# Kernel tuning notes

Hardware: AMD Instinct MI355X
Metric: run time of the kernel (lower is better)

Reference implementation:

```python
import jax, jax.numpy as jnp
import numpy as np

DT_RANK = 64
N_STATES = 16


def selective_scan(u, delta, A, B, C, D):
    # u,delta: [b,l,d]; A: [d,n]; B,C: [b,l,n]; D: [d]
    dA = jnp.einsum('bld,dn->bldn', delta, A)
    dB_u = jnp.einsum('bld,bld,bln->bldn', delta, u, B)
    # shifted exclusive suffix-sum: cum[t] = sum_{s=t+1}^{L-1} dA[s]
    dA_shift = jnp.concatenate([dA[:, 1:], jnp.zeros_like(dA[:, :1])], axis=1)
    dA_cumsum = jnp.exp(jnp.flip(jnp.cumsum(jnp.flip(dA_shift, axis=1), axis=1), axis=1))
    xs = jnp.cumsum(dB_u * dA_cumsum, axis=1) / (dA_cumsum + 1e-12)
    y = jnp.einsum('bldn,bln->bld', xs, C)
    return y + u * D


def setup_inputs() -> dict:
    key = jax.random.key(0)
    ks = jax.random.split(key, 6)
    b, l, d = 2, 1024, 1024
    dt_rank, n = DT_RANK, N_STATES
    x = jax.random.normal(ks[0], (b, l, d), dtype=jnp.float32)
    # Dense kernels with glorot-ish scale
    W_x = jax.random.normal(ks[1], (d, dt_rank + 2 * n), dtype=jnp.float32) * (1.0 / np.sqrt(d))
    W_dt = jax.random.normal(ks[2], (dt_rank, d), dtype=jnp.float32) * (1.0 / np.sqrt(dt_rank))
    b_dt = jnp.zeros((d,), dtype=jnp.float32)
    # A_log = log(repeat(1..n, d)) as in S6.__init__
    A_log = jnp.log(jnp.tile(jnp.arange(1, n + 1, dtype=jnp.float32)[None, :], (d, 1)))
    D = jnp.ones((d,), dtype=jnp.float32)
    W_out = jax.random.normal(ks[3], (d, d), dtype=jnp.float32) * (1.0 / np.sqrt(d))
    b_out = jnp.zeros((d,), dtype=jnp.float32)
    return {"x": x, "W_x": W_x, "W_dt": W_dt, "b_dt": b_dt,
            "A_log": A_log, "D": D, "W_out": W_out, "b_out": b_out}


def reference(x, W_x, W_dt, b_dt, A_log, D, W_out, b_out):
    n = A_log.shape[1]
    A = -jnp.exp(A_log)                     # [d,n]
    x_dbl = jnp.einsum('bld,de->ble', x, W_x)  # [b,l,dt_rank+2n]
    delta = x_dbl[..., :DT_RANK]
    B = x_dbl[..., DT_RANK:DT_RANK + n]
    C = x_dbl[..., DT_RANK + n:]
    delta = jax.nn.softplus(jnp.einsum('blr,rd->bld', delta, W_dt) + b_dt)
    y = selective_scan(x, delta, A, B, C, D)
    return jnp.einsum('bld,de->ble', y, W_out) + b_out
```

## Files before the change

kernel.cpp:

```cpp
#include <hip/hip_runtime.h>
#include <hip/hip_bf16.h>

#define LSEQ 1024
#define DMODEL 1024
#define NSTATE 16
#define DTRANK 64
#define ECOL 96
#define MTOT 2048

typedef short s16x8 __attribute__((ext_vector_type(8)));
typedef float f32x4 __attribute__((ext_vector_type(4)));

__device__ inline unsigned short f2bf(float f) {
    unsigned int u = __builtin_bit_cast(unsigned int, f);
    u += 0x7FFFu + ((u >> 16) & 1u);
    return (unsigned short)(u >> 16);
}
__device__ inline float bf2f(unsigned short h) {
    unsigned int u = ((unsigned int)h) << 16;
    return __builtin_bit_cast(float, u);
}

__device__ inline f32x4 shflup4(f32x4 v, int off) {
    f32x4 r;
    r[0] = __shfl_up(v[0], off, 64);
    r[1] = __shfl_up(v[1], off, 64);
    r[2] = __shfl_up(v[2], off, 64);
    r[3] = __shfl_up(v[3], off, 64);
    return r;
}

__global__ __launch_bounds__(256) void k_prep(const float* __restrict__ x,
                                              const float* __restrict__ Wx,
                                              const float* __restrict__ Wdt,
                                              const float* __restrict__ Wout,
                                              float* __restrict__ xT,
                                              unsigned short* __restrict__ xh,
                                              unsigned short* __restrict__ xl,
                                              unsigned short* __restrict__ WxTh,
                                              unsigned short* __restrict__ WxTl,
                                              unsigned short* __restrict__ WdtTh,
                                              unsigned short* __restrict__ WdtTl,
                                              unsigned short* __restrict__ WbfT) {
    __shared__ float t[64][65];
    int id = blockIdx.x;
    int tid = threadIdx.x;
    if (id < 512) {
        int d0 = (id & 15) * 64, m0 = (id >> 4) * 64;
        int tx = tid & 63, ty = tid >> 6;
#pragma unroll
        for (int j = 0; j < 64; j += 4) {
            size_t src = (size_t)(m0 + ty + j) * 1024 + d0 + tx;
            float v = x[src];
            t[ty + j][tx] = v;
            unsigned short h = f2bf(v);
            xh[src] = h;
            xl[src] = f2bf(v - bf2f(h));
        }
        __syncthreads();
#pragma unroll
        for (int j = 0; j < 64; j += 4)
            xT[(size_t)(d0 + ty + j) * 2048 + m0 + tx] = t[tx][ty + j];
    } else if (id < 512 + 96) {
        int id2 = id - 512;
        int e0 = (id2 % 3) * 32, k0 = (id2 / 3) * 32;
        int tx = tid & 31, ty = tid >> 5;
#pragma unroll
        for (int j = 0; j < 32; j += 8)
            t[ty + j][tx] = Wx[(size_t)(k0 + ty + j) * 96 + e0 + tx];
        __syncthreads();
#pragma unroll
        for (int j = 0; j < 32; j += 8) {
            float v = t[tx][ty + j];
            unsigned short h = f2bf(v);
            WxTh[(size_t)(e0 + ty + j) * 1024 + k0 + tx] = h;
            WxTl[(size_t)(e0 + ty + j) * 1024 + k0 + tx] = f2bf(v - bf2f(h));
        }
    } else if (id < 512 + 96 + 64) {
        int id3 = id - (512 + 96);
        int d0 = (id3 & 31) * 32, r0 = (id3 >> 5) * 32;
        int tx = tid & 31, ty = tid >> 5;
#pragma unroll
        for (int j = 0; j < 32; j += 8)
            t[ty + j][tx] = Wdt[(size_t)(r0 + ty + j) * 1024 + d0 + tx];
        __syncthreads();
#pragma unroll
        for (int j = 0; j < 32; j += 8) {
            float v = t[tx][ty + j];
            unsigned short h = f2bf(v);
            WdtTh[(size_t)(d0 + ty + j) * 64 + r0 + tx] = h;
            WdtTl[(size_t)(d0 + ty + j) * 64 + r0 + tx] = f2bf(v - bf2f(h));
        }
    } else {
        int id4 = id - (512 + 96 + 64);
        int e0 = (id4 & 15) * 64, k0 = (id4 >> 4) * 64;
        int tx = tid & 63, ty = tid >> 6;
#pragma unroll
        for (int j = 0; j < 64; j += 4)
            t[ty + j][tx] = Wout[(size_t)(k0 + ty + j) * 1024 + e0 + tx];
        __syncthreads();
#pragma unroll
        for (int j = 0; j < 64; j += 4)
            WbfT[(size_t)(e0 + ty + j) * 1024 + k0 + tx] = f2bf(t[tx][ty + j]);
    }
}

__global__ __launch_bounds__(256) void k_xdbl3(const unsigned short* __restrict__ xh,
                                               const unsigned short* __restrict__ xl,
                                               const unsigned short* __restrict__ WxTh,
                                               const unsigned short* __restrict__ WxTl,
                                               float* __restrict__ part) {
    __shared__ unsigned short Ah[32 * 64], Al[32 * 64];
    __shared__ unsigned short Bh[96 * 64], Bl[96 * 64];
    int bm = (blockIdx.x >> 2) * 32;
    int slice = blockIdx.x & 3;
    int tid = threadIdx.x, lane = tid & 63, w = tid >> 6;
    int wm = w >> 1, wn = w & 1;
    int r = lane & 15, kb = lane >> 4;

    f32x4 acc[3];
#pragma unroll
    for (int nf = 0; nf < 3; ++nf) acc[nf] = (f32x4){0.f, 0.f, 0.f, 0.f};

#pragma unroll 1
    for (int kc = 0; kc < 4; ++kc) {
        int kbase = slice * 256 + kc * 64;
        __syncthreads();
        {
            int row = tid >> 3, cc = tid & 7;
            size_t src = (size_t)(bm + row) * 1024 + kbase + cc * 8;
            int dstB = row * 128 + ((cc * 16) ^ ((row & 7) << 4));
            *(s16x8*)((char*)Ah + dstB) = *(const s16x8*)&xh[src];
            *(s16x8*)((char*)Al + dstB) = *(const s16x8*)&xl[src];
        }
#pragma unroll
        for (int j = 0; j < 3; ++j) {
            int c = tid + j * 256;
            int row = c >> 3, cc = c & 7;
            size_t src = (size_t)row * 1024 + kbase + cc * 8;
            int dstB = row * 128 + ((cc * 16) ^ ((row & 7) << 4));
            *(s16x8*)((char*)Bh + dstB) = *(const s16x8*)&WxTh[src];
            *(s16x8*)((char*)Bl + dstB) = *(const s16x8*)&WxTl[src];
        }
        __syncthreads();
#pragma unroll
        for (int ks = 0; ks < 2; ++ks) {
            int sw = (ks * 64 + kb * 16) ^ ((r & 7) << 4);
            s16x8 a_h = *(const s16x8*)((char*)Ah + (wm * 16 + r) * 128 + sw);
            s16x8 a_l = *(const s16x8*)((char*)Al + (wm * 16 + r) * 128 + sw);
#pragma unroll
            for (int nf = 0; nf < 3; ++nf) {
                int brow = wn * 48 + nf * 16 + r;
                s16x8 b_h = *(const s16x8*)((char*)Bh + brow * 128 + sw);
                s16x8 b_l = *(const s16x8*)((char*)Bl + brow * 128 + sw);
                acc[nf] = __builtin_amdgcn_mfma_f32_16x16x32_bf16(a_h, b_h, acc[nf], 0, 0, 0);
                acc[nf] = __builtin_amdgcn_mfma_f32_16x16x32_bf16(a_h, b_l, acc[nf], 0, 0, 0);
                acc[nf] = __builtin_amdgcn_mfma_f32_16x16x32_bf16(a_l, b_h, acc[nf], 0, 0, 0);
            }
        }
    }
    float* pb = part + (size_t)slice * 2048 * 96;
#pragma unroll
    for (int nf = 0; nf < 3; ++nf)
#pragma unroll
        for (int j = 0; j < 4; ++j)
            pb[(size_t)(bm + wm * 16 + kb * 4 + j) * 96 + wn * 48 + nf * 16 + r] = acc[nf][j];
}

__global__ __launch_bounds__(256) void k_delta2(const float* __restrict__ part,
                                                const unsigned short* __restrict__ WdtTh,
                                                const unsigned short* __restrict__ WdtTl,
                                                const float* __restrict__ bdt,
                                                float* __restrict__ deltaT,
                                                float* __restrict__ bpk,
                                                float* __restrict__ cpk) {
    __shared__ char pool[34816];
    unsigned short* Ah = (unsigned short*)pool;
    unsigned short* Al = (unsigned short*)(pool + 16384);
    float (*slab)[32][68] = (float (*)[32][68])pool;

    int bm = blockIdx.y * 128;
    int bn = blockIdx.x * 64;
    int tid = threadIdx.x, lane = tid & 63, w = tid >> 6;
    int wm = w >> 1, wn = w & 1;
    int r = lane & 15, kb = lane >> 4;

#pragma unroll
    for (int i = 0; i < 8; ++i) {
        int q = tid + i * 256;
        int row = q >> 4, c4 = q & 15;
        size_t off = (size_t)(bm + row) * 96 + c4 * 4;
        f32x4 v = *(const f32x4*)&part[off];
#pragma unroll
        for (int s = 1; s < 4; ++s) v += *(const f32x4*)&part[(size_t)s * 2048 * 96 + off];
        ushort4 h4, l4;
        h4.x = f2bf(v[0]); l4.x = f2bf(v[0] - bf2f(h4.x));
        h4.y = f2bf(v[1]); l4.y = f2bf(v[1] - bf2f(h4.y));
        h4.z = f2bf(v[2]); l4.z = f2bf(v[2] - bf2f(h4.z));
        h4.w = f2bf(v[3]); l4.w = f2bf(v[3] - bf2f(h4.w));
        int dstB = row * 128 + ((c4 * 8) ^ ((row & 7) << 4));
        *(ushort4*)((char*)Ah + dstB) = h4;
        *(ushort4*)((char*)Al + dstB) = l4;
    }
    if (blockIdx.x == 0) {
#pragma unroll
        for (int i = 0; i < 4; ++i) {
            int q = tid + i * 256;
            int row = q >> 3, c4 = q & 7;
            size_t off = (size_t)(bm + row) * 96 + 64 + c4 * 4;
            f32x4 v = *(const f32x4*)&part[off];
#pragma unroll
            for (int s = 1; s < 4; ++s) v += *(const f32x4*)&part[(size_t)s * 2048 * 96 + off];
            if (c4 < 4) *(f32x4*)&bpk[(size_t)(bm + row) * 16 + c4 * 4] = v;
            else        *(f32x4*)&cpk[(size_t)(bm + row) * 16 + (c4 - 4) * 4] = v;
        }
    }
    __syncthreads();

    f32x4 acc[4][2];
#pragma unroll
    for (int mf = 0; mf < 4; ++mf)
#pragma unroll
        for (int nf = 0; nf < 2; ++nf) acc[mf][nf] = (f32x4){0.f, 0.f, 0.f, 0.f};

#pragma unroll
    for (int ks = 0; ks < 2; ++ks) {
        int sw = (ks * 64 + kb * 16) ^ ((r & 7) << 4);
        s16x8 Afh[4], Afl[4], Bh[2], Bl[2];
#pragma unroll
        for (int mf = 0; mf < 4; ++mf) {
            int arow = wm * 64 + mf * 16 + r;
            Afh[mf] = *(const s16x8*)((char*)Ah + arow * 128 + sw);
            Afl[mf] = *(const s16x8*)((char*)Al + arow * 128 + sw);
        }
#pragma unroll
        for (int nf = 0; nf < 2; ++nf) {
            size_t b = (size_t)(bn + wn * 32 + nf * 16 + r) * 64 + ks * 32 + kb * 8;
            Bh[nf] = *(const s16x8*)&WdtTh[b];
            Bl[nf] = *(const s16x8*)&WdtTl[b];
        }
#pragma unroll
        for (int mf = 0; mf < 4; ++mf)
#pragma unroll
            for (int nf = 0; nf < 2; ++nf) {
                acc[mf][nf] = __builtin_amdgcn_mfma_f32_16x16x32_bf16(Afh[mf], Bh[nf], acc[mf][nf], 0, 0, 0);
                acc[mf][nf] = __builtin_amdgcn_mfma_f32_16x16x32_bf16(Afh[mf], Bl[nf], acc[mf][nf], 0, 0, 0);
                acc[mf][nf] = __builtin_amdgcn_mfma_f32_16x16x32_bf16(Afl[mf], Bh[nf], acc[mf][nf], 0, 0, 0);
            }
    }
    __syncthreads();

#pragma unroll
    for (int nf = 0; nf < 2; ++nf) {
        float bb = bdt[bn + wn * 32 + nf * 16 + r];
#pragma unroll
        for (int mf = 0; mf < 4; ++mf)
#pragma unroll
            for (int j = 0; j < 4; ++j) {
                float z = acc[mf][nf][j] + bb;
                float sp = fmaxf(z, 0.f) + log1pf(expf(-fabsf(z)));
                slab[w][nf * 16 + r][mf * 16 + kb * 4 + j] = sp;
            }
    }
#pragma unroll
    for (int i = 0; i < 8; ++i) {
        int idx = i * 64 + lane;
        int dl = idx >> 4, mq = (idx & 15) * 4;
        f32x4 v = *(const f32x4*)&slab[w][dl][mq];
        *(f32x4*)&deltaT[(size_t)(bn + wn * 32 + dl) * MTOT + bm + wm * 64 + mq] = v;
    }
}

__global__ __launch_bounds__(256) void k_scan3(const float* __restrict__ deltaT,
                                               const float* __restrict__ xT,
                                               const float* __restrict__ bpk,
                                               const float* __restrict__ cpk,
                                               const float* __restrict__ Alog,
                                               const float* __restrict__ Dp,
                                               unsigned short* __restrict__ yTbf) {
    __shared__ double csum[64];
    __shared__ double Rbef[64];
    __shared__ float TcL[64 * 20];
    __shared__ float syp[64 * 17];

    int tid = threadIdx.x;
    int c = tid >> 2, l = tid & 3;
    int w = tid >> 6, lane = tid & 63;
    int d = blockIdx.x & 1023, b = blockIdx.x >> 10;
    int m0 = b * 1024;

    const f32x4* dp = (const f32x4*)(deltaT + (size_t)d * MTOT + m0 + c * 16);
    const f32x4* up = (const f32x4*)(xT + (size_t)d * MTOT + m0 + c * 16);
    const f32x4* Bp = (const f32x4*)bpk + (size_t)(m0 + c * 16) * 4 + l;
    const f32x4* Cp = (const f32x4*)cpk + (size_t)(m0 + c * 16) * 4 + l;

    double dsum = 0.0;
#pragma unroll
    for (int i = 0; i < 4; ++i) {
        f32x4 v = dp[i];
        dsum += (double)v[0] + (double)v[1] + (double)v[2] + (double)v[3];
    }
    if (l == 0) csum[c] = dsum;
    __syncthreads();
    if (tid < 64) {
        double v = csum[tid];
#pragma unroll
        for (int off = 1; off < 64; off <<= 1) {
            double t = __shfl_down(v, off, 64);
            if (tid + off < 64) v += t;
        }
        Rbef[tid] = v;
    }
    __syncthreads();

    float Af[4], Sb[4];
    double Rb = Rbef[c];
#pragma unroll
    for (int j = 0; j < 4; ++j) {
        Af[j] = -__expf(Alog[d * NSTATE + 4 * l + j]);
        Sb[j] = (float)((double)Af[j] * Rb);
    }
    float Dv = Dp[d];

    float P = 0.f;
    f32x4 Tn = {0.f, 0.f, 0.f, 0.f};
#pragma unroll 1
    for (int t4 = 0; t4 < 4; ++t4) {
        f32x4 rdv = dp[t4];
        f32x4 ruv = up[t4];
        f32x4 Bq0 = Bp[(t4 * 4 + 0) * 4];
        f32x4 Bq1 = Bp[(t4 * 4 + 1) * 4];
        f32x4 Bq2 = Bp[(t4 * 4 + 2) * 4];
        f32x4 Bq3 = Bp[(t4 * 4 + 3) * 4];
        f32x4 Bq[4] = {Bq0, Bq1, Bq2, Bq3};
#pragma unroll
        for (int k = 0; k < 4; ++k) {
            float dlt = rdv[k];
            P += dlt;
            float du = dlt * ruv[k];
#pragma unroll
            for (int j = 0; j < 4; ++j) {
                float e = __expf(fmaf(-Af[j], P, Sb[j]));
                Tn[j] = fmaf(du * Bq[k][j], e, Tn[j]);
            }
        }
    }
    *(f32x4*)&TcL[c * 20 + 4 * l] = Tn;
    __syncthreads();

    {
        f32x4 v = *(const f32x4*)&TcL[lane * 20 + 4 * w];
#pragma unroll
        for (int off = 1; off < 64; off <<= 1) {
            f32x4 t = shflup4(v, off);
            if (lane >= off) v += t;
        }
        f32x4 ex = shflup4(v, 1);
        if (lane == 0) ex = (f32x4){0.f, 0.f, 0.f, 0.f};
        *(f32x4*)&TcL[lane * 20 + 4 * w] = ex;
    }
    __syncthreads();
    f32x4 num = *(const f32x4*)&TcL[c * 20 + 4 * l];

    P = 0.f;
#pragma unroll 1
    for (int t4 = 0; t4 < 4; ++t4) {
        f32x4 rdv = dp[t4];
        f32x4 ruv = up[t4];
        f32x4 Bq[4], Cq[4];
#pragma unroll
        for (int k = 0; k < 4; ++k) {
            Bq[k] = Bp[(t4 * 4 + k) * 4];
            Cq[k] = Cp[(t4 * 4 + k) * 4];
        }
#pragma unroll
        for (int k = 0; k < 4; ++k) {
            float dlt = rdv[k];
            P += dlt;
            float du = dlt * ruv[k];
            float psum = 0.f;
#pragma unroll
            for (int j = 0; j < 4; ++j) {
                float e = __expf(fmaf(-Af[j], P, Sb[j]));
                num[j] = fmaf(du * Bq[k][j], e, num[j]);
                float rr = __builtin_amdgcn_rcpf(e + 1e-12f);
                psum = fmaf(num[j] * rr, Cq[k][j], psum);
            }
            psum += __shfl_xor(psum, 1);
            psum += __shfl_xor(psum, 2);
            if (l == 0) syp[c * 17 + t4 * 4 + k] = fmaf(ruv[k], Dv, psum);
        }
    }
    __syncthreads();
    {
        int cc = tid >> 2, oo = (tid & 3) * 4;
        const float* sp = &syp[cc * 17 + oo];
        ushort4 o;
        o.x = f2bf(sp[0]);
        o.y = f2bf(sp[1]);
        o.z = f2bf(sp[2]);
        o.w = f2bf(sp[3]);
        *reinterpret_cast<ushort4*>(&yTbf[(size_t)d * MTOT + m0 + tid * 4]) = o;
    }
}

__global__ __launch_bounds__(256) void k_ytr(const unsigned short* __restrict__ in,
                                             unsigned short* __restrict__ out) {
    __shared__ unsigned short t[64][66];
    int d0 = blockIdx.y * 64, m0 = blockIdx.x * 64;
    int tx = threadIdx.x & 63, ty = threadIdx.x >> 6;
#pragma unroll
    for (int j = 0; j < 64; j += 4)
        t[ty + j][tx] = in[(size_t)(d0 + ty + j) * MTOT + m0 + tx];
    __syncthreads();
#pragma unroll
    for (int j = 0; j < 64; j += 4)
        out[(size_t)(m0 + ty + j) * 1024 + d0 + tx] = t[tx][ty + j];
}

__global__ __launch_bounds__(256) void k_gemm(const unsigned short* __restrict__ A,
                                              const unsigned short* __restrict__ B,
                                              const float* __restrict__ bias,
                                              float* __restrict__ out) {
    __shared__ unsigned short As[64 * 64];
    __shared__ unsigned short Bs[64 * 64];
    const int GN = 1024, GK = 1024;
    int bm = blockIdx.y * 64;
    int bn = blockIdx.x * 64;
    int tid = threadIdx.x;
    int lane = tid & 63;
    int w = tid >> 6;
    int wm = w >> 1, wn = w & 1;
    int r = lane & 15, kb = lane >> 4;

    f32x4 acc[2][2];
#pragma unroll
    for (int mf = 0; mf < 2; ++mf)
#pragma unroll
        for (int nf = 0; nf < 2; ++nf) acc[mf][nf] = (f32x4){0.f, 0.f, 0.f, 0.f};

    s16x8 ra[2], rb[2];
    auto stage_load = [&](int k0) {
#pragma unroll
        for (int i = 0; i < 2; ++i) {
            int q = tid + i * 256;
            ra[i] = *reinterpret_cast<const s16x8*>(&A[(size_t)(bm + (q >> 3)) * GK + k0 + (q & 7) * 8]);
            rb[i] = *reinterpret_cast<const s16x8*>(&B[(size_t)(bn + (q >> 3)) * GK + k0 + (q & 7) * 8]);
        }
    };

    stage_load(0);
    for (int k0 = 0; k0 < GK; k0 += 64) {
        __syncthreads();
#pragma unroll
        for (int i = 0; i < 2; ++i) {
            int q = tid + i * 256;
            int row = q >> 3;
            int dstB = row * 128 + (((q & 7) * 16) ^ ((row & 7) << 4));
            *(s16x8*)((char*)As + dstB) = ra[i];
            *(s16x8*)((char*)Bs + dstB) = rb[i];
        }
        __syncthreads();
        if (k0 + 64 < GK) stage_load(k0 + 64);
#pragma unroll
        for (int ks = 0; ks < 2; ++ks) {
            int sw = (ks * 64 + kb * 16) ^ ((r & 7) << 4);
            s16x8 af[2], bfr[2];
#pragma unroll
            for (int mf = 0; mf < 2; ++mf)
                af[mf] = *(const s16x8*)((char*)As + (wm * 32 + mf * 16 + r) * 128 + sw);
#pragma unroll
            for (int nf = 0; nf < 2; ++nf)
                bfr[nf] = *(const s16x8*)((char*)Bs + (wn * 32 + nf * 16 + r) * 128 + sw);
#pragma unroll
            for (int mf = 0; mf < 2; ++mf)
#pragma unroll
                for (int nf = 0; nf < 2; ++nf)
                    acc[mf][nf] = __builtin_amdgcn_mfma_f32_16x16x32_bf16(af[mf], bfr[nf], acc[mf][nf], 0, 0, 0);
        }
    }
#pragma unroll
    for (int nf = 0; nf < 2; ++nf) {
        float bb = bias[bn + wn * 32 + nf * 16 + r];
#pragma unroll
        for (int mf = 0; mf < 2; ++mf)
#pragma unroll
            for (int j = 0; j < 4; ++j)
                out[(size_t)(bm + wm * 32 + mf * 16 + kb * 4 + j) * GN + bn + wn * 32 + nf * 16 + r] =
                    acc[mf][nf][j] + bb;
    }
}

extern "C" void kernel_launch(void* const* d_in, const int* in_sizes, int n_in,
                              void* d_out, int out_size, void* d_ws, size_t ws_size,
                              hipStream_t stream) {
    const float* x    = (const float*)d_in[0];
    const float* Wx   = (const float*)d_in[1];
    const float* Wdt  = (const float*)d_in[2];
    const float* bdt  = (const float*)d_in[3];
    const float* Alog = (const float*)d_in[4];
    const float* Dp   = (const float*)d_in[5];
    const float* Wout = (const float*)d_in[6];
    const float* bout = (const float*)d_in[7];
    float* out = (float*)d_out;

    float* xT     = (float*)d_ws;
    float* deltaT = xT + 1024 * 2048;
    float* bpk    = deltaT + 1024 * 2048;
    float* cpk    = bpk + 2048 * 16;
    float* part   = cpk + 2048 * 16;
    unsigned short* xh    = (unsigned short*)(part + 4 * 2048 * 96);
    unsigned short* xl    = xh + 2048 * 1024;
    unsigned short* WxTh  = xl + 2048 * 1024;
    unsigned short* WxTl  = WxTh + 96 * 1024;
    unsigned short* WdtTh = WxTl + 96 * 1024;
    unsigned short* WdtTl = WdtTh + 1024 * 64;
    unsigned short* yTbf  = WdtTl + 1024 * 64;
    unsigned short* ybf   = yTbf + 1024 * 2048;
    unsigned short* WbfT  = ybf + 2048 * 1024;

    k_prep<<<928, 256, 0, stream>>>(x, Wx, Wdt, Wout, xT, xh, xl,
                                    WxTh, WxTl, WdtTh, WdtTl, WbfT);
    k_xdbl3<<<256, 256, 0, stream>>>(xh, xl, WxTh, WxTl, part);
    k_delta2<<<dim3(16, 16), 256, 0, stream>>>(part, WdtTh, WdtTl, bdt, deltaT, bpk, cpk);
    k_scan3<<<2048, 256, 0, stream>>>(deltaT, xT, bpk, cpk, Alog, Dp, yTbf);
    k_ytr<<<dim3(32, 16), 256, 0, stream>>>(yTbf, ybf);
    k_gemm<<<dim3(16, 32), 256, 0, stream>>>(ybf, WbfT, bout, out);
}
```

Before: 72.13 us.

## Process four channels per scan block, store transposed x as bf16, split x on the fly

```diff
diff --git a/kernel.cpp b/kernel.cpp
--- a/kernel.cpp
+++ b/kernel.cpp
@@ -34,9 +34,7 @@
                                               const float* __restrict__ Wx,
                                               const float* __restrict__ Wdt,
                                               const float* __restrict__ Wout,
-                                              float* __restrict__ xT,
-                                              unsigned short* __restrict__ xh,
-                                              unsigned short* __restrict__ xl,
+                                              unsigned short* __restrict__ xTbf,
                                               unsigned short* __restrict__ WxTh,
                                               unsigned short* __restrict__ WxTl,
                                               unsigned short* __restrict__ WdtTh,
@@ -49,18 +47,12 @@
         int d0 = (id & 15) * 64, m0 = (id >> 4) * 64;
         int tx = tid & 63, ty = tid >> 6;
 #pragma unroll
-        for (int j = 0; j < 64; j += 4) {
-            size_t src = (size_t)(m0 + ty + j) * 1024 + d0 + tx;
-            float v = x[src];
-            t[ty + j][tx] = v;
-            unsigned short h = f2bf(v);
-            xh[src] = h;
-            xl[src] = f2bf(v - bf2f(h));
-        }
-        __syncthreads();
-#pragma unroll
         for (int j = 0; j < 64; j += 4)
-            xT[(size_t)(d0 + ty + j) * 2048 + m0 + tx] = t[tx][ty + j];
+            t[ty + j][tx] = x[(size_t)(m0 + ty + j) * 1024 + d0 + tx];
+        __syncthreads();
+#pragma unroll
+        for (int j = 0; j < 64; j += 4)
+            xTbf[(size_t)(d0 + ty + j) * 2048 + m0 + tx] = f2bf(t[tx][ty + j]);
     } else if (id < 512 + 96) {
         int id2 = id - 512;
         int e0 = (id2 % 3) * 32, k0 = (id2 / 3) * 32;
@@ -105,8 +97,7 @@
     }
 }
 
-__global__ __launch_bounds__(256) void k_xdbl3(const unsigned short* __restrict__ xh,
-                                               const unsigned short* __restrict__ xl,
+__global__ __launch_bounds__(256) void k_xdbl3(const float* __restrict__ x,
                                                const unsigned short* __restrict__ WxTh,
                                                const unsigned short* __restrict__ WxTl,
                                                float* __restrict__ part) {
@@ -129,9 +120,19 @@
         {
             int row = tid >> 3, cc = tid & 7;
             size_t src = (size_t)(bm + row) * 1024 + kbase + cc * 8;
+            float4 v0 = *(const float4*)&x[src];
+            float4 v1 = *(const float4*)&x[src + 4];
+            float vv[8] = {v0.x, v0.y, v0.z, v0.w, v1.x, v1.y, v1.z, v1.w};
+            s16x8 h, lo;
+#pragma unroll
+            for (int j = 0; j < 8; ++j) {
+                unsigned short hb = f2bf(vv[j]);
+                h[j] = (short)hb;
+                lo[j] = (short)f2bf(vv[j] - bf2f(hb));
+            }
             int dstB = row * 128 + ((cc * 16) ^ ((row & 7) << 4));
-            *(s16x8*)((char*)Ah + dstB) = *(const s16x8*)&xh[src];
-            *(s16x8*)((char*)Al + dstB) = *(const s16x8*)&xl[src];
+            *(s16x8*)((char*)Ah + dstB) = h;
+            *(s16x8*)((char*)Al + dstB) = lo;
         }
 #pragma unroll
         for (int j = 0; j < 3; ++j) {
@@ -271,85 +272,108 @@
     }
 }
 
-__global__ __launch_bounds__(256) void k_scan3(const float* __restrict__ deltaT,
-                                               const float* __restrict__ xT,
+__global__ __launch_bounds__(256) void k_scan4(const float* __restrict__ deltaT,
+                                               const unsigned short* __restrict__ xTbf,
                                                const float* __restrict__ bpk,
                                                const float* __restrict__ cpk,
                                                const float* __restrict__ Alog,
                                                const float* __restrict__ Dp,
                                                unsigned short* __restrict__ yTbf) {
-    __shared__ double csum[64];
-    __shared__ double Rbef[64];
-    __shared__ float TcL[64 * 20];
-    __shared__ float syp[64 * 17];
+    __shared__ double csum[64][4];
+    __shared__ double Rbef[64][4];
+    __shared__ float TcL[64][4][4][4];
+    __shared__ float syp[4][64 * 17];
 
     int tid = threadIdx.x;
     int c = tid >> 2, l = tid & 3;
     int w = tid >> 6, lane = tid & 63;
-    int d = blockIdx.x & 1023, b = blockIdx.x >> 10;
+    int dgrp = blockIdx.x & 255, b = blockIdx.x >> 8;
+    int d0 = dgrp * 4;
     int m0 = b * 1024;
 
-    const f32x4* dp = (const f32x4*)(deltaT + (size_t)d * MTOT + m0 + c * 16);
-    const f32x4* up = (const f32x4*)(xT + (size_t)d * MTOT + m0 + c * 16);
+    const f32x4* dp[4];
+    const unsigned short* up[4];
+#pragma unroll
+    for (int dg = 0; dg < 4; ++dg) {
+        dp[dg] = (const f32x4*)(deltaT + (size_t)(d0 + dg) * MTOT + m0 + c * 16);
+        up[dg] = xTbf + (size_t)(d0 + dg) * MTOT + m0 + c * 16;
+    }
+
+#pragma unroll
+    for (int dg = 0; dg < 4; ++dg) {
+        double s = 0.0;
+#pragma unroll
+        for (int i = 0; i < 4; ++i) {
+            f32x4 v = dp[dg][i];
+            s += (double)v[0] + (double)v[1] + (double)v[2] + (double)v[3];
+        }
+        if (l == 0) csum[c][dg] = s;
+    }
+    __syncthreads();
+    {
+        double v = csum[lane][w];
+#pragma unroll
+        for (int off = 1; off < 64; off <<= 1) {
+            double t = __shfl_down(v, off, 64);
+            if (lane + off < 64) v += t;
+        }
+        Rbef[lane][w] = v;
+    }
+    __syncthreads();
+
+    float Af[4][4], Sb[4][4];
+#pragma unroll
+    for (int dg = 0; dg < 4; ++dg) {
+        double Rb = Rbef[c][dg];
+#pragma unroll
+        for (int j = 0; j < 4; ++j) {
+            Af[dg][j] = -__expf(Alog[(d0 + dg) * NSTATE + 4 * l + j]);
+            Sb[dg][j] = (float)((double)Af[dg][j] * Rb);
+        }
+    }
+
     const f32x4* Bp = (const f32x4*)bpk + (size_t)(m0 + c * 16) * 4 + l;
     const f32x4* Cp = (const f32x4*)cpk + (size_t)(m0 + c * 16) * 4 + l;
 
-    double dsum = 0.0;
-#pragma unroll
-    for (int i = 0; i < 4; ++i) {
-        f32x4 v = dp[i];
-        dsum += (double)v[0] + (double)v[1] + (double)v[2] + (double)v[3];
-    }
-    if (l == 0) csum[c] = dsum;
-    __syncthreads();
-    if (tid < 64) {
-        double v = csum[tid];
-#pragma unroll
-        for (int off = 1; off < 64; off <<= 1) {
-            double t = __shfl_down(v, off, 64);
-            if (tid + off < 64) v += t;
-        }
-        Rbef[tid] = v;
-    }
-    __syncthreads();
-
-    float Af[4], Sb[4];
-    double Rb = Rbef[c];
-#pragma unroll
-    for (int j = 0; j < 4; ++j) {
-        Af[j] = -__expf(Alog[d * NSTATE + 4 * l + j]);
-        Sb[j] = (float)((double)Af[j] * Rb);
-    }
-    float Dv = Dp[d];
-
-    float P = 0.f;
-    f32x4 Tn = {0.f, 0.f, 0.f, 0.f};
+    float P[4] = {0.f, 0.f, 0.f, 0.f};
+    f32x4 Tn[4];
+#pragma unroll
+    for (int dg = 0; dg < 4; ++dg) Tn[dg] = (f32x4){0.f, 0.f, 0.f, 0.f};
 #pragma unroll 1
     for (int t4 = 0; t4 < 4; ++t4) {
-        f32x4 rdv = dp[t4];
-        f32x4 ruv = up[t4];
-        f32x4 Bq0 = Bp[(t4 * 4 + 0) * 4];
-        f32x4 Bq1 = Bp[(t4 * 4 + 1) * 4];
-        f32x4 Bq2 = Bp[(t4 * 4 + 2) * 4];
-        f32x4 Bq3 = Bp[(t4 * 4 + 3) * 4];
-        f32x4 Bq[4] = {Bq0, Bq1, Bq2, Bq3};
-#pragma unroll
-        for (int k = 0; k < 4; ++k) {
-            float dlt = rdv[k];
-            P += dlt;
-            float du = dlt * ruv[k];
-#pragma unroll
-            for (int j = 0; j < 4; ++j) {
-                float e = __expf(fmaf(-Af[j], P, Sb[j]));
-                Tn[j] = fmaf(du * Bq[k][j], e, Tn[j]);
-            }
-        }
-    }
-    *(f32x4*)&TcL[c * 20 + 4 * l] = Tn;
-    __syncthreads();
-
-    {
-        f32x4 v = *(const f32x4*)&TcL[lane * 20 + 4 * w];
+        f32x4 Bq[4];
+#pragma unroll
+        for (int k = 0; k < 4; ++k) Bq[k] = Bp[(t4 * 4 + k) * 4];
+        f32x4 rdv[4];
+        float ru[4][4];
+#pragma unroll
+        for (int dg = 0; dg < 4; ++dg) {
+            rdv[dg] = dp[dg][t4];
+            ushort4 uv = *(const ushort4*)(up[dg] + t4 * 4);
+            ru[dg][0] = bf2f(uv.x); ru[dg][1] = bf2f(uv.y);
+            ru[dg][2] = bf2f(uv.z); ru[dg][3] = bf2f(uv.w);
+        }
+#pragma unroll
+        for (int k = 0; k < 4; ++k)
+#pragma unroll
+            for (int dg = 0; dg < 4; ++dg) {
+                float dlt = rdv[dg][k];
+                P[dg] += dlt;
+                float du = dlt * ru[dg][k];
+#pragma unroll
+                for (int j = 0; j < 4; ++j) {
+                    float e = __expf(fmaf(-Af[dg][j], P[dg], Sb[dg][j]));
+                    Tn[dg][j] = fmaf(du * Bq[k][j], e, Tn[dg][j]);
+                }
+            }
+    }
+#pragma unroll
+    for (int dg = 0; dg < 4; ++dg) *(f32x4*)&TcL[c][dg][l][0] = Tn[dg];
+    __syncthreads();
+
+#pragma unroll
+    for (int l2 = 0; l2 < 4; ++l2) {
+        f32x4 v = *(const f32x4*)&TcL[lane][w][l2][0];
 #pragma unroll
         for (int off = 1; off < 64; off <<= 1) {
             f32x4 t = shflup4(v, off);
@@ -357,50 +381,75 @@
         }
         f32x4 ex = shflup4(v, 1);
         if (lane == 0) ex = (f32x4){0.f, 0.f, 0.f, 0.f};
-        *(f32x4*)&TcL[lane * 20 + 4 * w] = ex;
-    }
-    __syncthreads();
-    f32x4 num = *(const f32x4*)&TcL[c * 20 + 4 * l];
-
-    P = 0.f;
+        *(f32x4*)&TcL[lane][w][l2][0] = ex;
+    }
+    __syncthreads();
+
+    f32x4 num[4];
+#pragma unroll
+    for (int dg = 0; dg < 4; ++dg) num[dg] = *(const f32x4*)&TcL[c][dg][l][0];
+
+    float Dv[4];
+#pragma unroll
+    for (int dg = 0; dg < 4; ++dg) { Dv[dg] = Dp[d0 + dg]; P[dg] = 0.f; }
+
 #pragma unroll 1
     for (int t4 = 0; t4 < 4; ++t4) {
-        f32x4 rdv = dp[t4];
-        f32x4 ruv = up[t4];
         f32x4 Bq[4], Cq[4];
 #pragma unroll
         for (int k = 0; k < 4; ++k) {
             Bq[k] = Bp[(t4 * 4 + k) * 4];
             Cq[k] = Cp[(t4 * 4 + k) * 4];
         }
+        f32x4 rdv[4];
+        float ru[4][4];
+#pragma unroll
+        for (int dg = 0; dg < 4; ++dg) {
+            rdv[dg] = dp[dg][t4];
+            ushort4 uv = *(const ushort4*)(up[dg] + t4 * 4);
+            ru[dg][0] = bf2f(uv.x); ru[dg][1] = bf2f(uv.y);
+            ru[dg][2] = bf2f(uv.z); ru[dg][3] = bf2f(uv.w);
+        }
 #pragma unroll
         for (int k = 0; k < 4; ++k) {
-            float dlt = rdv[k];
-            P += dlt;
-            float du = dlt * ruv[k];
-            float psum = 0.f;
-#pragma unroll
-            for (int j = 0; j < 4; ++j) {
-                float e = __expf(fmaf(-Af[j], P, Sb[j]));
-                num[j] = fmaf(du * Bq[k][j], e, num[j]);
-                float rr = __builtin_amdgcn_rcpf(e + 1e-12f);
-                psum = fmaf(num[j] * rr, Cq[k][j], psum);
-            }
-            psum += __shfl_xor(psum, 1);
-            psum += __shfl_xor(psum, 2);
-            if (l == 0) syp[c * 17 + t4 * 4 + k] = fmaf(ruv[k], Dv, psum);
+            float psum[4];
+#pragma unroll
+            for (int dg = 0; dg < 4; ++dg) {
+                float dlt = rdv[dg][k];
+                P[dg] += dlt;
+                float du = dlt * ru[dg][k];
+                float ps = 0.f;
+#pragma unroll
+                for (int j = 0; j < 4; ++j) {
+                    float e = __expf(fmaf(-Af[dg][j], P[dg], Sb[dg][j]));
+                    num[dg][j] = fmaf(du * Bq[k][j], e, num[dg][j]);
+                    float rr = __builtin_amdgcn_rcpf(e + 1e-12f);
+                    ps = fmaf(num[dg][j] * rr, Cq[k][j], ps);
+                }
+                psum[dg] = ps;
+            }
+#pragma unroll
+            for (int dg = 0; dg < 4; ++dg) {
+                float ps = psum[dg];
+                ps += __shfl_xor(ps, 1);
+                ps += __shfl_xor(ps, 2);
+                if (l == 0) syp[dg][c * 17 + t4 * 4 + k] = fmaf(ru[dg][k], Dv[dg], ps);
+            }
         }
     }
     __syncthreads();
     {
         int cc = tid >> 2, oo = (tid & 3) * 4;
-        const float* sp = &syp[cc * 17 + oo];
-        ushort4 o;
-        o.x = f2bf(sp[0]);
-        o.y = f2bf(sp[1]);
-        o.z = f2bf(sp[2]);
-        o.w = f2bf(sp[3]);
-        *reinterpret_cast<ushort4*>(&yTbf[(size_t)d * MTOT + m0 + tid * 4]) = o;
+#pragma unroll
+        for (int dg = 0; dg < 4; ++dg) {
+            const float* sp = &syp[dg][cc * 17 + oo];
+            ushort4 o;
+            o.x = f2bf(sp[0]);
+            o.y = f2bf(sp[1]);
+            o.z = f2bf(sp[2]);
+            o.w = f2bf(sp[3]);
+            *reinterpret_cast<ushort4*>(&yTbf[(size_t)(d0 + dg) * MTOT + m0 + tid * 4]) = o;
+        }
     }
 }
 
@@ -504,14 +553,12 @@
     const float* bout = (const float*)d_in[7];
     float* out = (float*)d_out;
 
-    float* xT     = (float*)d_ws;
-    float* deltaT = xT + 1024 * 2048;
+    float* deltaT = (float*)d_ws;
     float* bpk    = deltaT + 1024 * 2048;
     float* cpk    = bpk + 2048 * 16;
     float* part   = cpk + 2048 * 16;
-    unsigned short* xh    = (unsigned short*)(part + 4 * 2048 * 96);
-    unsigned short* xl    = xh + 2048 * 1024;
-    unsigned short* WxTh  = xl + 2048 * 1024;
+    unsigned short* xTbf  = (unsigned short*)(part + 4 * 2048 * 96);
+    unsigned short* WxTh  = xTbf + 1024 * 2048;
     unsigned short* WxTl  = WxTh + 96 * 1024;
     unsigned short* WdtTh = WxTl + 96 * 1024;
     unsigned short* WdtTl = WdtTh + 1024 * 64;
@@ -519,11 +566,11 @@
     unsigned short* ybf   = yTbf + 1024 * 2048;
     unsigned short* WbfT  = ybf + 2048 * 1024;
 
-    k_prep<<<928, 256, 0, stream>>>(x, Wx, Wdt, Wout, xT, xh, xl,
+    k_prep<<<928, 256, 0, stream>>>(x, Wx, Wdt, Wout, xTbf,
                                     WxTh, WxTl, WdtTh, WdtTl, WbfT);
-    k_xdbl3<<<256, 256, 0, stream>>>(xh, xl, WxTh, WxTl, part);
+    k_xdbl3<<<256, 256, 0, stream>>>(x, WxTh, WxTl, part);
     k_delta2<<<dim3(16, 16), 256, 0, stream>>>(part, WdtTh, WdtTl, bdt, deltaT, bpk, cpk);
-    k_scan3<<<2048, 256, 0, stream>>>(deltaT, xT, bpk, cpk, Alog, Dp, yTbf);
+    k_scan4<<<512, 256, 0, stream>>>(deltaT, xTbf, bpk, cpk, Alog, Dp, yTbf);
     k_ytr<<<dim3(32, 16), 256, 0, stream>>>(yTbf, ybf);
     k_gemm<<<dim3(16, 32), 256, 0, stream>>>(ybf, WbfT, bout, out);
 }
```

Result: slower. 80.63 us (+11.8%).

## Store transposed x as bf16, split x in-GEMM, use exp2 in scan

Applied to the files above, without the earlier changes.

```diff
diff --git a/kernel.cpp b/kernel.cpp
--- a/kernel.cpp
+++ b/kernel.cpp
@@ -10,6 +10,13 @@
 
 typedef short s16x8 __attribute__((ext_vector_type(8)));
 typedef float f32x4 __attribute__((ext_vector_type(4)));
+
+#if __has_builtin(__builtin_amdgcn_exp2f)
+#define EXP2F(x) __builtin_amdgcn_exp2f(x)
+#else
+#define EXP2F(x) exp2f(x)
+#endif
+#define LOG2E 1.4426950408889634
 
 __device__ inline unsigned short f2bf(float f) {
     unsigned int u = __builtin_bit_cast(unsigned int, f);
@@ -34,9 +41,7 @@
                                               const float* __restrict__ Wx,
                                               const float* __restrict__ Wdt,
                                               const float* __restrict__ Wout,
-                                              float* __restrict__ xT,
-                                              unsigned short* __restrict__ xh,
-                                              unsigned short* __restrict__ xl,
+                                              unsigned short* __restrict__ xTbf,
                                               unsigned short* __restrict__ WxTh,
                                               unsigned short* __restrict__ WxTl,
                                               unsigned short* __restrict__ WdtTh,
@@ -49,18 +54,12 @@
         int d0 = (id & 15) * 64, m0 = (id >> 4) * 64;
         int tx = tid & 63, ty = tid >> 6;
 #pragma unroll
-        for (int j = 0; j < 64; j += 4) {
-            size_t src = (size_t)(m0 + ty + j) * 1024 + d0 + tx;
-            float v = x[src];
-            t[ty + j][tx] = v;
-            unsigned short h = f2bf(v);
-            xh[src] = h;
-            xl[src] = f2bf(v - bf2f(h));
-        }
-        __syncthreads();
-#pragma unroll
         for (int j = 0; j < 64; j += 4)
-            xT[(size_t)(d0 + ty + j) * 2048 + m0 + tx] = t[tx][ty + j];
+            t[ty + j][tx] = x[(size_t)(m0 + ty + j) * 1024 + d0 + tx];
+        __syncthreads();
+#pragma unroll
+        for (int j = 0; j < 64; j += 4)
+            xTbf[(size_t)(d0 + ty + j) * 2048 + m0 + tx] = f2bf(t[tx][ty + j]);
     } else if (id < 512 + 96) {
         int id2 = id - 512;
         int e0 = (id2 % 3) * 32, k0 = (id2 / 3) * 32;
@@ -105,8 +104,7 @@
     }
 }
 
-__global__ __launch_bounds__(256) void k_xdbl3(const unsigned short* __restrict__ xh,
-                                               const unsigned short* __restrict__ xl,
+__global__ __launch_bounds__(256) void k_xdbl3(const float* __restrict__ x,
                                                const unsigned short* __restrict__ WxTh,
                                                const unsigned short* __restrict__ WxTl,
                                                float* __restrict__ part) {
@@ -129,9 +127,19 @@
         {
             int row = tid >> 3, cc = tid & 7;
             size_t src = (size_t)(bm + row) * 1024 + kbase + cc * 8;
+            float4 v0 = *(const float4*)&x[src];
+            float4 v1 = *(const float4*)&x[src + 4];
+            float vv[8] = {v0.x, v0.y, v0.z, v0.w, v1.x, v1.y, v1.z, v1.w};
+            s16x8 h, lo;
+#pragma unroll
+            for (int j = 0; j < 8; ++j) {
+                unsigned short hb = f2bf(vv[j]);
+                h[j] = (short)hb;
+                lo[j] = (short)f2bf(vv[j] - bf2f(hb));
+            }
             int dstB = row * 128 + ((cc * 16) ^ ((row & 7) << 4));
-            *(s16x8*)((char*)Ah + dstB) = *(const s16x8*)&xh[src];
-            *(s16x8*)((char*)Al + dstB) = *(const s16x8*)&xl[src];
+            *(s16x8*)((char*)Ah + dstB) = h;
+            *(s16x8*)((char*)Al + dstB) = lo;
         }
 #pragma unroll
         for (int j = 0; j < 3; ++j) {
@@ -272,7 +280,7 @@
 }
 
 __global__ __launch_bounds__(256) void k_scan3(const float* __restrict__ deltaT,
-                                               const float* __restrict__ xT,
+                                               const unsigned short* __restrict__ xTbf,
                                                const float* __restrict__ bpk,
                                                const float* __restrict__ cpk,
                                                const float* __restrict__ Alog,
@@ -290,7 +298,7 @@
     int m0 = b * 1024;
 
     const f32x4* dp = (const f32x4*)(deltaT + (size_t)d * MTOT + m0 + c * 16);
-    const f32x4* up = (const f32x4*)(xT + (size_t)d * MTOT + m0 + c * 16);
+    const unsigned short* up = xTbf + (size_t)d * MTOT + m0 + c * 16;
     const f32x4* Bp = (const f32x4*)bpk + (size_t)(m0 + c * 16) * 4 + l;
     const f32x4* Cp = (const f32x4*)cpk + (size_t)(m0 + c * 16) * 4 + l;
 
@@ -313,12 +321,14 @@
     }
     __syncthreads();
 
-    float Af[4], Sb[4];
+    float Af2[4], Sb2[4];
     double Rb = Rbef[c];
 #pragma unroll
     for (int j = 0; j < 4; ++j) {
-        Af[j] = -__expf(Alog[d * NSTATE + 4 * l + j]);
-        Sb[j] = (float)((double)Af[j] * Rb);
+        float Af = -__expf(Alog[d * NSTATE + 4 * l + j]);
+        double A2 = (double)Af * LOG2E;
+        Af2[j] = (float)A2;
+        Sb2[j] = (float)(A2 * Rb);
     }
     float Dv = Dp[d];
 
@@ -327,20 +337,19 @@
 #pragma unroll 1
     for (int t4 = 0; t4 < 4; ++t4) {
         f32x4 rdv = dp[t4];
-        f32x4 ruv = up[t4];
-        f32x4 Bq0 = Bp[(t4 * 4 + 0) * 4];
-        f32x4 Bq1 = Bp[(t4 * 4 + 1) * 4];
-        f32x4 Bq2 = Bp[(t4 * 4 + 2) * 4];
-        f32x4 Bq3 = Bp[(t4 * 4 + 3) * 4];
-        f32x4 Bq[4] = {Bq0, Bq1, Bq2, Bq3};
+        ushort4 uv = *(const ushort4*)(up + t4 * 4);
+        float ru[4] = {bf2f(uv.x), bf2f(uv.y), bf2f(uv.z), bf2f(uv.w)};
+        f32x4 Bq[4];
+#pragma unroll
+        for (int k = 0; k < 4; ++k) Bq[k] = Bp[(t4 * 4 + k) * 4];
 #pragma unroll
         for (int k = 0; k < 4; ++k) {
             float dlt = rdv[k];
             P += dlt;
-            float du = dlt * ruv[k];
+            float du = dlt * ru[k];
 #pragma unroll
             for (int j = 0; j < 4; ++j) {
-                float e = __expf(fmaf(-Af[j], P, Sb[j]));
+                float e = EXP2F(fmaf(-Af2[j], P, Sb2[j]));
                 Tn[j] = fmaf(du * Bq[k][j], e, Tn[j]);
             }
         }
@@ -366,7 +375,8 @@
 #pragma unroll 1
     for (int t4 = 0; t4 < 4; ++t4) {
         f32x4 rdv = dp[t4];
-        f32x4 ruv = up[t4];
+        ushort4 uv = *(const ushort4*)(up + t4 * 4);
+        float ru[4] = {bf2f(uv.x), bf2f(uv.y), bf2f(uv.z), bf2f(uv.w)};
         f32x4 Bq[4], Cq[4];
 #pragma unroll
         for (int k = 0; k < 4; ++k) {
@@ -377,18 +387,18 @@
         for (int k = 0; k < 4; ++k) {
             float dlt = rdv[k];
             P += dlt;
-            float du = dlt * ruv[k];
+            float du = dlt * ru[k];
             float psum = 0.f;
 #pragma unroll
             for (int j = 0; j < 4; ++j) {
-                float e = __expf(fmaf(-Af[j], P, Sb[j]));
+                float e = EXP2F(fmaf(-Af2[j], P, Sb2[j]));
                 num[j] = fmaf(du * Bq[k][j], e, num[j]);
                 float rr = __builtin_amdgcn_rcpf(e + 1e-12f);
                 psum = fmaf(num[j] * rr, Cq[k][j], psum);
             }
             psum += __shfl_xor(psum, 1);
             psum += __shfl_xor(psum, 2);
-            if (l == 0) syp[c * 17 + t4 * 4 + k] = fmaf(ruv[k], Dv, psum);
+            if (l == 0) syp[c * 17 + t4 * 4 + k] = fmaf(ru[k], Dv, psum);
         }
     }
     __syncthreads();
@@ -504,14 +514,12 @@
     const float* bout = (const float*)d_in[7];
     float* out = (float*)d_out;
 
-    float* xT     = (float*)d_ws;
-    float* deltaT = xT + 1024 * 2048;
+    float* deltaT = (float*)d_ws;
     float* bpk    = deltaT + 1024 * 2048;
     float* cpk    = bpk + 2048 * 16;
     float* part   = cpk + 2048 * 16;
-    unsigned short* xh    = (unsigned short*)(part + 4 * 2048 * 96);
-    unsigned short* xl    = xh + 2048 * 1024;
-    unsigned short* WxTh  = xl + 2048 * 1024;
+    unsigned short* xTbf  = (unsigned short*)(part + 4 * 2048 * 96);
+    unsigned short* WxTh  = xTbf + 1024 * 2048;
     unsigned short* WxTl  = WxTh + 96 * 1024;
     unsigned short* WdtTh = WxTl + 96 * 1024;
     unsigned short* WdtTl = WdtTh + 1024 * 64;
@@ -519,11 +527,11 @@
     unsigned short* ybf   = yTbf + 1024 * 2048;
     unsigned short* WbfT  = ybf + 2048 * 1024;
 
-    k_prep<<<928, 256, 0, stream>>>(x, Wx, Wdt, Wout, xT, xh, xl,
+    k_prep<<<928, 256, 0, stream>>>(x, Wx, Wdt, Wout, xTbf,
                                     WxTh, WxTl, WdtTh, WdtTl, WbfT);
-    k_xdbl3<<<256, 256, 0, stream>>>(xh, xl, WxTh, WxTl, part);
+    k_xdbl3<<<256, 256, 0, stream>>>(x, WxTh, WxTl, part);
     k_delta2<<<dim3(16, 16), 256, 0, stream>>>(part, WdtTh, WdtTl, bdt, deltaT, bpk, cpk);
-    k_scan3<<<2048, 256, 0, stream>>>(deltaT, xT, bpk, cpk, Alog, Dp, yTbf);
+    k_scan3<<<2048, 256, 0, stream>>>(deltaT, xTbf, bpk, cpk, Alog, Dp, yTbf);
     k_ytr<<<dim3(32, 16), 256, 0, stream>>>(yTbf, ybf);
     k_gemm<<<dim3(16, 32), 256, 0, stream>>>(ybf, WbfT, bout, out);
 }
```

Result: slower. 75.74 us (+5.0%).
